# Optimization experiments

Measured on AMD Instinct MI355X. Metric: run time of the kernel, lower is better.

## Reference

```python
import jax, jax.numpy as jnp
import numpy as np

LR = 1e-4   # learning_rate from init
EPS = 1e-8


def setup_inputs() -> dict:
    key = jax.random.key(0)
    k1, k2 = jax.random.split(key)
    N, K, F = 8192, 8192, 4096
    return {
        "x": jax.random.normal(k1, (N, F), jnp.float32),
        "centroids": jax.random.normal(k2, (K, F), jnp.float32),
        "m": jnp.zeros((K,), jnp.float32),
        "v": jnp.zeros((K,), jnp.float32),
        "betas": jnp.array([0.9, 0.999, 1.0, 1.0], jnp.float32),
        "step": 1,
    }


def reference(x, centroids, m, v, betas, step):
    N = x.shape[0]
    K = centroids.shape[0]
    dt = x.dtype
    # dist[k, n] = ||x_n - c_k||^2, via norm expansion (same math as sum((x-c)^2))
    xn = jnp.sum(x * x, axis=1)                    # [N]
    cn = jnp.sum(centroids * centroids, axis=1)    # [K]
    dist = cn[:, None] + xn[None, :] - 2.0 * (centroids @ x.T)  # [K, N]
    nearest = jnp.argmin(dist, axis=0)             # [N]
    # point_loss = sum(dist[:, nearest]) / N ; sum over K of gathered cols == gather of colsums
    colsum = jnp.sum(dist, axis=0)                 # [N]
    point_loss = jnp.sum(colsum[nearest]) / N
    # sum_{i,j} ||c_i - c_j||^2 = 2K*sum||c||^2 - 2*||sum_i c_i||^2 (includes zero diagonal)
    csum = jnp.sum(centroids, axis=0)
    centroid_loss = 1.0 / (2.0 * K * jnp.sum(cn) - 2.0 * jnp.sum(csum * csum))
    # per-cluster segment reduce replaces the Python loop over K
    counts = jax.ops.segment_sum(jnp.ones((N,), dt), nearest, num_segments=K)  # [K]
    sums = jax.ops.segment_sum(x, nearest, num_segments=K)                     # [K, F]
    nonempty = counts > 0
    new_center = sums / jnp.maximum(counts, 1.0)[:, None]
    delta = jnp.where(nonempty, jnp.sum((new_center - centroids) ** 2, axis=1), 0.0)  # [K]
    delta_k = jnp.sum(nonempty.astype(dt))
    sum_delta = jnp.sum(delta)
    # Adam-style per-cluster state update (only for non-empty clusters)
    g = delta + betas[2] * point_loss + betas[3] * centroid_loss
    m_new = jnp.where(nonempty, betas[0] * m + (1.0 - betas[0]) * g, m)
    v_new = jnp.where(nonempty, betas[1] * v + (1.0 - betas[1]) * g * g, v)
    mh = m_new / (1.0 - betas[0] ** step)
    vh = v_new / (1.0 - betas[1] ** step)
    upd = LR * mh / (jnp.sqrt(vh) + EPS)
    next_centroids = jnp.where(nonempty[:, None], centroids - upd[:, None], centroids)
    return sum_delta / delta_k, point_loss, centroid_loss, next_centroids, m_new, v_new
```

## Files before the change

kernel.cpp:

```cpp
#include <hip/hip_runtime.h>
#include <stdint.h>

#define KCL 8192
#define NPT 8192
#define FD  4096
#define KF  33554432
#define LRC 1e-4f
#define EPSC 1e-8f
#define SLAB 1024
#define BK  32

typedef float  f32x4 __attribute__((ext_vector_type(4)));
typedef __fp16 h8    __attribute__((ext_vector_type(8)));
typedef __fp16 h4    __attribute__((ext_vector_type(4)));

struct Scal {
  float Scn;
  float csum2;
  float cl;
  float pl_sum;
  float sum_delta;
  int   nonempty;
};

__device__ __forceinline__ void gload16(const void* g, void* l) {
  __builtin_amdgcn_global_load_lds((const __attribute__((address_space(1))) void*)g,
                                   (__attribute__((address_space(3))) void*)l, 16, 0, 0);
}

__device__ __forceinline__ float wave_sum(float v) {
  #pragma unroll
  for (int m = 1; m < 64; m <<= 1) v += __shfl_xor(v, m, 64);
  return v;
}
__device__ __forceinline__ double wave_sum(double v) {
  #pragma unroll
  for (int m = 1; m < 64; m <<= 1) v += __shfl_xor(v, m, 64);
  return v;
}

__global__ __launch_bounds__(256) void rownorm_k(const float* __restrict__ src,
                                                 double* __restrict__ norms) {
  __shared__ double sred[4];
  const int r = blockIdx.x, t = threadIdx.x;
  const f32x4* row = (const f32x4*)(src + (size_t)r * FD);
  double ss = 0.0;
  #pragma unroll
  for (int q = 0; q < 4; ++q) {
    f32x4 v = row[q * 256 + t];
    ss += (double)(v[0]*v[0] + v[1]*v[1]) + (double)(v[2]*v[2] + v[3]*v[3]);
  }
  ss = wave_sum(ss);
  int wave = t >> 6, lane = t & 63;
  if (lane == 0) sred[wave] = ss;
  __syncthreads();
  if (t == 0) norms[r] = sred[0] + sred[1] + sred[2] + sred[3];
}

template<bool WITH_DOT>
__global__ __launch_bounds__(256) void prep_rows(
    const float* __restrict__ src, __fp16* __restrict__ hi, __fp16* __restrict__ lo,
    const float* __restrict__ csum, float* __restrict__ colsum, const Scal* __restrict__ sc)
{
  __shared__ double sred[4], sred2[4];
  const int r = blockIdx.x, t = threadIdx.x;
  const size_t rb = (size_t)r * FD;
  const f32x4* row = (const f32x4*)(src + rb);
  double ss = 0.0, dd = 0.0;
  #pragma unroll
  for (int q = 0; q < 4; ++q) {
    int c4 = q * 256 + t;
    f32x4 v = row[c4];
    h4 hv = __builtin_convertvector(v, h4);
    f32x4 hb = __builtin_convertvector(hv, f32x4);
    h4 lv = __builtin_convertvector(v - hb, h4);
    *(h4*)(hi + rb + (size_t)c4 * 4) = hv;
    *(h4*)(lo + rb + (size_t)c4 * 4) = lv;
    if (WITH_DOT) {
      ss += (double)(v[0]*v[0] + v[1]*v[1]) + (double)(v[2]*v[2] + v[3]*v[3]);
      f32x4 cs = *(const f32x4*)(csum + c4 * 4);
      dd += (double)(v[0]*cs[0] + v[1]*cs[1]) + (double)(v[2]*cs[2] + v[3]*cs[3]);
    }
  }
  if (WITH_DOT) {
    ss = wave_sum(ss); dd = wave_sum(dd);
    int wave = t >> 6, lane = t & 63;
    if (lane == 0) { sred[wave] = ss; sred2[wave] = dd; }
    __syncthreads();
    if (t == 0) {
      double S = sred[0] + sred[1] + sred[2] + sred[3];
      double D = sred2[0] + sred2[1] + sred2[2] + sred2[3];
      colsum[r] = (float)((double)sc->Scn + (double)KCL * S - 2.0 * D);
    }
  }
}

__global__ __launch_bounds__(256) void csum_part_k(const float* __restrict__ c,
                                                   float* __restrict__ parts) {
  int f = blockIdx.x * 256 + threadIdx.x;
  int r0 = blockIdx.y * 256;
  float s = 0.f;
  for (int i = 0; i < 256; ++i) s += c[(size_t)(r0 + i) * FD + f];
  parts[(size_t)blockIdx.y * FD + f] = s;
}

__global__ __launch_bounds__(256) void csum_reduce_k(const float* __restrict__ parts,
                                                     float* __restrict__ csum, Scal* sc) {
  int f = blockIdx.x * 256 + threadIdx.x;
  float s = 0.f;
  for (int j = 0; j < 32; ++j) s += parts[(size_t)j * FD + f];
  csum[f] = s;
  float sq = wave_sum(s * s);
  __shared__ float sr[4];
  int wave = threadIdx.x >> 6, lane = threadIdx.x & 63;
  if (lane == 0) sr[wave] = sq;
  __syncthreads();
  if (threadIdx.x == 0) atomicAdd(&sc->csum2, sr[0] + sr[1] + sr[2] + sr[3]);
}

__global__ __launch_bounds__(256) void cn_reduce_k(const double* __restrict__ cn, Scal* sc) {
  double s = 0.0;
  for (int i = threadIdx.x; i < KCL; i += 256) s += cn[i];
  s = wave_sum(s);
  __shared__ double sr[4];
  int wave = threadIdx.x >> 6, lane = threadIdx.x & 63;
  if (lane == 0) sr[wave] = s;
  __syncthreads();
  if (threadIdx.x == 0) {
    double S = sr[0] + sr[1] + sr[2] + sr[3];
    sc->Scn = (float)S;
    sc->cl = (float)(1.0 / (2.0 * (double)KCL * S - 2.0 * (double)sc->csum2));
  }
}

__global__ __launch_bounds__(512, 2) void gemm_argmin_k(
    const __fp16* __restrict__ Ahi, const __fp16* __restrict__ Alo,
    const __fp16* __restrict__ Bhi, const __fp16* __restrict__ Blo,
    const double* __restrict__ cn,
    double* __restrict__ part_val, int* __restrict__ part_idx,
    int kglob0, int nglob0, int swz)
{
  __shared__ __fp16 tile[2 * 4 * 8192];

  const int tid  = threadIdx.x;
  const int lane = tid & 63;
  const int w    = tid >> 6;
  const int wr   = w >> 2, wc = w & 3;
  const int ln15 = lane & 15, lc = lane >> 4;

  int kb, nb;
  if (swz) {
    int l = (blockIdx.x & 7) * 128 + (blockIdx.x >> 3);
    kb = l & 31; nb = l >> 5;
  } else {
    kb = blockIdx.y; nb = blockIdx.x;
  }
  const int k0l = kb * 256, n0l = nb * 256;
  const int k0g = kglob0 + k0l, n0g = nglob0 + n0l;

  const __fp16* gAh = Ahi + (size_t)k0l * FD;
  const __fp16* gAl = Alo + (size_t)k0l * FD;
  const __fp16* gBh = Bhi + (size_t)n0l * FD;
  const __fp16* gBl = Blo + (size_t)n0l * FD;

  const int c0 = tid,        r0 = c0 >> 2, sc0 = (c0 & 3) ^ ((r0 >> 1) & 3);
  const int c1 = tid + 512,  r1 = c1 >> 2, sc1 = (c1 & 3) ^ ((r1 >> 1) & 3);
  const size_t gof0 = (size_t)r0 * FD + sc0 * 8;
  const size_t gof1 = (size_t)r1 * FD + sc1 * 8;

  #define TBUF(buf, arr) (tile + (((buf) * 4 + (arr)) << 13))
  #define STAGE(gsrc, buf, arr, fo) do { \
    gload16((gsrc) + gof0 + (fo), TBUF(buf, arr) + c0 * 8); \
    gload16((gsrc) + gof1 + (fo), TBUF(buf, arr) + c1 * 8); } while (0)

  const int pcs = (lc ^ ((ln15 >> 1) & 3)) * 8;
  const int abase = wr * 128 + ln15;
  const int bbase = wc * 64 + ln15;

  f32x4 acc[8][4] = {};
  h8 ah[8], bh[4];

  STAGE(gAh, 0, 0, 0); STAGE(gBh, 0, 2, 0); STAGE(gAl, 0, 1, 0); STAGE(gBl, 0, 3, 0);
  asm volatile("s_waitcnt vmcnt(0)" ::: "memory");
  __builtin_amdgcn_s_barrier();

  for (int t = 0; t < FD / BK; ++t) {
    const int cur = t & 1, nxt = cur ^ 1;
    const size_t fo = (size_t)(t + 1) * BK;
    const bool st = (t < FD / BK - 1);

    {
      const __fp16* sA = TBUF(cur, 0);
      const __fp16* sB = TBUF(cur, 2);
      #pragma unroll
      for (int m = 0; m < 8; ++m) ah[m] = *(const h8*)(sA + (abase + m * 16) * 32 + pcs);
      #pragma unroll
      for (int n = 0; n < 4; ++n) bh[n] = *(const h8*)(sB + (bbase + n * 16) * 32 + pcs);
    }
    if (st) STAGE(gAh, nxt, 0, fo);
    __builtin_amdgcn_s_barrier();
    __builtin_amdgcn_s_setprio(1);
    #pragma unroll
    for (int m = 0; m < 8; ++m)
      #pragma unroll
      for (int n = 0; n < 4; ++n)
        acc[m][n] = __builtin_amdgcn_mfma_f32_16x16x32_f16(ah[m], bh[n], acc[m][n], 0, 0, 0);
    __builtin_amdgcn_s_setprio(0);
    asm volatile("s_waitcnt vmcnt(2)" ::: "memory");
    __builtin_amdgcn_sched_barrier(0);
    __builtin_amdgcn_s_barrier();

    {
      h8 bl[4];
      const __fp16* sB = TBUF(cur, 3);
      #pragma unroll
      for (int n = 0; n < 4; ++n) bl[n] = *(const h8*)(sB + (bbase + n * 16) * 32 + pcs);
      if (st) STAGE(gBh, nxt, 2, fo);
      __builtin_amdgcn_s_barrier();
      __builtin_amdgcn_s_setprio(1);
      #pragma unroll
      for (int m = 0; m < 8; ++m)
        #pragma unroll
        for (int n = 0; n < 4; ++n)
          acc[m][n] = __builtin_amdgcn_mfma_f32_16x16x32_f16(ah[m], bl[n], acc[m][n], 0, 0, 0);
      __builtin_amdgcn_s_setprio(0);
      __builtin_amdgcn_s_barrier();
    }

    {
      h8 al[8];
      const __fp16* sA = TBUF(cur, 1);
      #pragma unroll
      for (int m = 0; m < 8; ++m) al[m] = *(const h8*)(sA + (abase + m * 16) * 32 + pcs);
      if (st) { STAGE(gAl, nxt, 1, fo); STAGE(gBl, nxt, 3, fo); }
      __builtin_amdgcn_s_barrier();
      __builtin_amdgcn_s_setprio(1);
      #pragma unroll
      for (int m = 0; m < 8; ++m)
        #pragma unroll
        for (int n = 0; n < 4; ++n)
          acc[m][n] = __builtin_amdgcn_mfma_f32_16x16x32_f16(al[m], bh[n], acc[m][n], 0, 0, 0);
      __builtin_amdgcn_s_setprio(0);
      asm volatile("s_waitcnt vmcnt(4)" ::: "memory");
      __builtin_amdgcn_sched_barrier(0);
      __builtin_amdgcn_s_barrier();
    }
  }

  double* eCn = (double*)tile;
  double* eV  = (double*)(tile + 1024);
  int*    eI  = (int*)(tile + 3072);
  __syncthreads();
  if (tid < 256) eCn[tid] = cn[k0g + tid];
  __syncthreads();

  #pragma unroll
  for (int n = 0; n < 4; ++n) {
    double bv = 1e300; int bi = 0x7fffffff;
    #pragma unroll
    for (int m = 0; m < 8; ++m)
      #pragma unroll
      for (int j = 0; j < 4; ++j) {
        int kl = wr * 128 + m * 16 + lc * 4 + j;
        double d = eCn[kl] - 2.0 * (double)acc[m][n][j];
        if (d < bv || (d == bv && kl < bi)) { bv = d; bi = kl; }
      }
    #pragma unroll
    for (int mask = 16; mask < 64; mask <<= 1) {
      double ov = __shfl_xor(bv, mask, 64);
      int    oi = __shfl_xor(bi, mask, 64);
      if (ov < bv || (ov == bv && oi < bi)) { bv = ov; bi = oi; }
    }
    if (lc == 0) {
      int col = wc * 64 + n * 16 + ln15;
      eV[wr * 256 + col] = bv; eI[wr * 256 + col] = bi;
    }
  }
  __syncthreads();
  if (tid < 256) {
    double v0 = eV[tid]; int i0 = eI[tid];
    double v1 = eV[256 + tid]; int i1 = eI[256 + tid];
    if (v1 < v0 || (v1 == v0 && i1 < i0)) { v0 = v1; i0 = i1; }
    part_val[(size_t)(k0g >> 8) * NPT + n0g + tid] = v0;
    part_idx[(size_t)(k0g >> 8) * NPT + n0g + tid] = i0 + k0g;
  }
  #undef TBUF
  #undef STAGE
}

__global__ __launch_bounds__(256) void nearest_k(
    const double* __restrict__ part_val, const int* __restrict__ part_idx,
    const float* __restrict__ colsum, int* __restrict__ nearest,
    int* __restrict__ counts, Scal* sc)
{
  int n = blockIdx.x * 256 + threadIdx.x;
  double bv = 1e300; int bi = 0x7fffffff;
  for (int kb = 0; kb < 32; ++kb) {
    double v = part_val[(size_t)kb * NPT + n];
    int    i = part_idx[(size_t)kb * NPT + n];
    if (v < bv || (v == bv && i < bi)) { bv = v; bi = i; }
  }
  nearest[n] = bi;
  atomicAdd(&counts[bi], 1);
  float pls = wave_sum(colsum[bi]);
  __shared__ float sr[4];
  int wave = threadIdx.x >> 6, lane = threadIdx.x & 63;
  if (lane == 0) sr[wave] = pls;
  __syncthreads();
  if (threadIdx.x == 0) atomicAdd(&sc->pl_sum, sr[0] + sr[1] + sr[2] + sr[3]);
}

__global__ __launch_bounds__(256) void scan_k(const int* __restrict__ counts,
                                              int* __restrict__ offsets) {
  __shared__ int s[256];
  int t = threadIdx.x;
  int base = t * 32;
  int sum = 0;
  for (int i = 0; i < 32; ++i) sum += counts[base + i];
  s[t] = sum; __syncthreads();
  for (int off = 1; off < 256; off <<= 1) {
    int v = (t >= off) ? s[t - off] : 0;
    __syncthreads();
    s[t] += v;
    __syncthreads();
  }
  int run = s[t] - sum;
  for (int i = 0; i < 32; ++i) { offsets[base + i] = run; run += counts[base + i]; }
}

__global__ __launch_bounds__(256) void fill_k(const int* __restrict__ nearest,
                                              const int* __restrict__ offsets,
                                              int* __restrict__ cursor, int* __restrict__ list) {
  int n = blockIdx.x * 256 + threadIdx.x;
  int k = nearest[n];
  int p = atomicAdd(&cursor[k], 1);
  list[offsets[k] + p] = n;
}

__global__ __launch_bounds__(256) void cluster_k(
    const float* __restrict__ x, const float* __restrict__ cen,
    const int* __restrict__ counts, const int* __restrict__ offsets,
    const int* __restrict__ list, float* __restrict__ delta, Scal* sc)
{
  int k = blockIdx.x, t = threadIdx.x;
  int cnt = counts[k];
  if (cnt == 0) { if (t == 0) delta[k] = 0.f; return; }
  f32x4 acc[4] = {};
  int off = offsets[k];
  for (int i = 0; i < cnt; ++i) {
    int n = list[off + i];
    const f32x4* row = (const f32x4*)(x + (size_t)n * FD);
    #pragma unroll
    for (int q = 0; q < 4; ++q) acc[q] += row[q * 256 + t];
  }
  const f32x4* crow = (const f32x4*)(cen + (size_t)k * FD);
  float part = 0.f;
  float fc = (float)cnt;
  #pragma unroll
  for (int q = 0; q < 4; ++q) {
    f32x4 c4 = crow[q * 256 + t];
    #pragma unroll
    for (int j = 0; j < 4; ++j) {
      float d = acc[q][j] / fc - c4[j];
      part += d * d;
    }
  }
  part = wave_sum(part);
  __shared__ float sr[4];
  int wave = t >> 6, lane = t & 63;
  if (lane == 0) sr[wave] = part;
  __syncthreads();
  if (t == 0) {
    float dsum = sr[0] + sr[1] + sr[2] + sr[3];
    delta[k] = dsum;
    atomicAdd(&sc->sum_delta, dsum);
    atomicAdd(&sc->nonempty, 1);
  }
}

__global__ __launch_bounds__(256) void adam_k(
    const float* __restrict__ m_in, const float* __restrict__ v_in,
    const float* __restrict__ betas, const int* __restrict__ step,
    const int* __restrict__ counts, const float* __restrict__ delta,
    const Scal* __restrict__ sc, float* __restrict__ out, float* __restrict__ upd)
{
  int k = blockIdx.x * 256 + threadIdx.x;
  float b0 = betas[0], b1 = betas[1], b2 = betas[2], b3 = betas[3];
  float pl = sc->pl_sum / (float)NPT;
  float cl = sc->cl;
  bool ne = counts[k] > 0;
  float g = delta[k] + b2 * pl + b3 * cl;
  float mn = ne ? (b0 * m_in[k] + (1.f - b0) * g) : m_in[k];
  float vn = ne ? (b1 * v_in[k] + (1.f - b1) * g * g) : v_in[k];
  int st = *step;
  float mh = mn / (1.f - powf(b0, (float)st));
  float vh = vn / (1.f - powf(b1, (float)st));
  float u = LRC * mh / (sqrtf(vh) + EPSC);
  upd[k] = ne ? u : 0.f;
  out[3 + (size_t)KF + k] = mn;
  out[3 + (size_t)KF + KCL + k] = vn;
  if (k == 0) {
    out[0] = sc->sum_delta / (float)sc->nonempty;
    out[1] = pl;
    out[2] = cl;
  }
}

__global__ __launch_bounds__(256) void nextc_k(const float* __restrict__ cen,
                                               const float* __restrict__ upd,
                                               float* __restrict__ out) {
  int i4 = blockIdx.x * 256 + threadIdx.x;
  f32x4 c = *(const f32x4*)(cen + (size_t)i4 * 4);
  float u = upd[i4 >> 10];
  float* o = out + 3 + (size_t)i4 * 4;
  o[0] = c[0] - u; o[1] = c[1] - u; o[2] = c[2] - u; o[3] = c[3] - u;
}

extern "C" void kernel_launch(void* const* d_in, const int* in_sizes, int n_in,
                              void* d_out, int out_size, void* d_ws, size_t ws_size,
                              hipStream_t stream) {
  const float* x     = (const float*)d_in[0];
  const float* cen   = (const float*)d_in[1];
  const float* m_in  = (const float*)d_in[2];
  const float* v_in  = (const float*)d_in[3];
  const float* betas = (const float*)d_in[4];
  const int*   step  = (const int*)d_in[5];
  float* out = (float*)d_out;

  char* p = (char*)d_ws;
  auto alloc = [&](size_t b) { char* r = p; p += (b + 255) & ~(size_t)255; return r; };
  Scal* sc      = (Scal*)alloc(sizeof(Scal));
  int* counts   = (int*)alloc(KCL * 4);
  int* cursor   = (int*)alloc(KCL * 4);
  size_t zlen   = (size_t)(p - (char*)d_ws);
  int* offsets  = (int*)alloc(KCL * 4);
  int* list     = (int*)alloc(NPT * 4);
  int* nearest  = (int*)alloc(NPT * 4);
  double* cn    = (double*)alloc(KCL * 8);
  float* colsum = (float*)alloc(NPT * 4);
  float* delta  = (float*)alloc(KCL * 4);
  float* upd    = (float*)alloc(KCL * 4);
  float* csum   = (float*)alloc(FD * 4);
  float* cparts = (float*)alloc(32 * FD * 4);
  double* pval  = (double*)alloc((size_t)32 * NPT * 8);
  int*   pidx   = (int*)alloc((size_t)32 * NPT * 4);
  const bool fast = ws_size >= (size_t)280 * 1024 * 1024;
  const size_t splitRows = fast ? (size_t)KCL : (size_t)SLAB;
  __fp16* chi = (__fp16*)alloc(splitRows * FD * 2);
  __fp16* clo = (__fp16*)alloc(splitRows * FD * 2);
  __fp16* xhi = (__fp16*)alloc(splitRows * FD * 2);
  __fp16* xlo = (__fp16*)alloc(splitRows * FD * 2);
  (void)in_sizes; (void)n_in; (void)out_size;

  hipMemsetAsync(d_ws, 0, zlen, stream);

  rownorm_k<<<KCL, 256, 0, stream>>>(cen, cn);
  csum_part_k<<<dim3(16, 32), 256, 0, stream>>>(cen, cparts);
  csum_reduce_k<<<16, 256, 0, stream>>>(cparts, csum, sc);
  cn_reduce_k<<<1, 256, 0, stream>>>(cn, sc);

  if (fast) {
    prep_rows<false><<<KCL, 256, 0, stream>>>(cen, chi, clo, nullptr, nullptr, nullptr);
    prep_rows<true><<<NPT, 256, 0, stream>>>(x, xhi, xlo, csum, colsum, sc);
    gemm_argmin_k<<<1024, 512, 0, stream>>>(chi, clo, xhi, xlo, cn, pval, pidx, 0, 0, 1);
  } else {
    for (int q = 0; q < NPT / SLAB; ++q) {
      prep_rows<true><<<SLAB, 256, 0, stream>>>(x + (size_t)q * SLAB * FD, xhi, xlo,
                                                csum, colsum + q * SLAB, sc);
      for (int pp = 0; pp < KCL / SLAB; ++pp) {
        prep_rows<false><<<SLAB, 256, 0, stream>>>(cen + (size_t)pp * SLAB * FD, chi, clo,
                                                   nullptr, nullptr, nullptr);
        gemm_argmin_k<<<dim3(SLAB / 256, SLAB / 256), 512, 0, stream>>>(
            chi, clo, xhi, xlo, cn, pval, pidx, pp * SLAB, q * SLAB, 0);
      }
    }
  }

  nearest_k<<<NPT / 256, 256, 0, stream>>>(pval, pidx, colsum, nearest, counts, sc);
  scan_k<<<1, 256, 0, stream>>>(counts, offsets);
  fill_k<<<NPT / 256, 256, 0, stream>>>(nearest, offsets, cursor, list);
  cluster_k<<<KCL, 256, 0, stream>>>(x, cen, counts, offsets, list, delta, sc);
  adam_k<<<KCL / 256, 256, 0, stream>>>(m_in, v_in, betas, step, counts, delta, sc, out, upd);
  nextc_k<<<KF / 4 / 256, 256, 0, stream>>>(cen, upd, out);
}
```

Measured before the change: 1.801 ms.

## Use 32x32 MFMA in GEMM, fuse centroid prep and cluster/Adam/update kernels

Switches the split-fp16 GEMM from 16x16x32 to 32x32x16 MFMA tiles, which lowers LDS fragment reads per flop and simplifies the argmin cross-lane reduction. It also fuses centroid row norms, column partial sums and the hi/lo fp16 split into a single pass over the centroids. The cluster mean, Adam update and next-centroid write are merged into one per-cluster kernel, removing the delta/upd buffers and two extra passes over 128MB. The price is a larger accumulator layout per wave, a more serial 32-row loop per block in the prep kernel, and an extra tiny finalize launch.

```diff
diff --git a/kernel.cpp b/kernel.cpp
--- a/kernel.cpp
+++ b/kernel.cpp
@@ -10,9 +10,10 @@
 #define SLAB 1024
 #define BK  32
 
-typedef float  f32x4 __attribute__((ext_vector_type(4)));
-typedef __fp16 h8    __attribute__((ext_vector_type(8)));
-typedef __fp16 h4    __attribute__((ext_vector_type(4)));
+typedef float  f32x4  __attribute__((ext_vector_type(4)));
+typedef float  f32x16 __attribute__((ext_vector_type(16)));
+typedef __fp16 h8     __attribute__((ext_vector_type(8)));
+typedef __fp16 h4     __attribute__((ext_vector_type(4)));
 
 struct Scal {
   float Scn;
@@ -37,6 +38,41 @@
   #pragma unroll
   for (int m = 1; m < 64; m <<= 1) v += __shfl_xor(v, m, 64);
   return v;
+}
+
+__global__ __launch_bounds__(256) void prep_cen_k(
+    const float* __restrict__ src, __fp16* __restrict__ hi, __fp16* __restrict__ lo,
+    double* __restrict__ norms, float* __restrict__ parts)
+{
+  __shared__ double snorm[32][4];
+  const int t = threadIdx.x;
+  const int wv = t >> 6, lane = t & 63;
+  const int rbase = blockIdx.x * 32;
+  f32x4 cs[4] = {};
+  for (int r = 0; r < 32; ++r) {
+    const size_t rb = (size_t)(rbase + r) * FD;
+    const f32x4* row = (const f32x4*)(src + rb);
+    double ss = 0.0;
+    #pragma unroll
+    for (int q = 0; q < 4; ++q) {
+      int c4i = q * 256 + t;
+      f32x4 v = row[c4i];
+      h4 hv = __builtin_convertvector(v, h4);
+      f32x4 hb = __builtin_convertvector(hv, f32x4);
+      h4 lv = __builtin_convertvector(v - hb, h4);
+      *(h4*)(hi + rb + (size_t)c4i * 4) = hv;
+      *(h4*)(lo + rb + (size_t)c4i * 4) = lv;
+      ss += (double)(v[0]*v[0] + v[1]*v[1]) + (double)(v[2]*v[2] + v[3]*v[3]);
+      cs[q] += v;
+    }
+    double wsum = wave_sum(ss);
+    if (lane == 0) snorm[r][wv] = wsum;
+  }
+  __syncthreads();
+  if (t < 32) norms[rbase + t] = snorm[t][0] + snorm[t][1] + snorm[t][2] + snorm[t][3];
+  #pragma unroll
+  for (int q = 0; q < 4; ++q)
+    *(f32x4*)(parts + (size_t)blockIdx.x * FD + (size_t)(q * 256 + t) * 4) = cs[q];
 }
 
 __global__ __launch_bounds__(256) void rownorm_k(const float* __restrict__ src,
@@ -105,10 +141,11 @@
 }
 
 __global__ __launch_bounds__(256) void csum_reduce_k(const float* __restrict__ parts,
-                                                     float* __restrict__ csum, Scal* sc) {
+                                                     float* __restrict__ csum, Scal* sc,
+                                                     int nparts) {
   int f = blockIdx.x * 256 + threadIdx.x;
   float s = 0.f;
-  for (int j = 0; j < 32; ++j) s += parts[(size_t)j * FD + f];
+  for (int j = 0; j < nparts; ++j) s += parts[(size_t)j * FD + f];
   csum[f] = s;
   float sq = wave_sum(s * s);
   __shared__ float sr[4];
@@ -146,7 +183,7 @@
   const int lane = tid & 63;
   const int w    = tid >> 6;
   const int wr   = w >> 2, wc = w & 3;
-  const int ln15 = lane & 15, lc = lane >> 4;
+  const int l31  = lane & 31, l5 = lane >> 5;
 
   int kb, nb;
   if (swz) {
@@ -173,12 +210,15 @@
     gload16((gsrc) + gof0 + (fo), TBUF(buf, arr) + c0 * 8); \
     gload16((gsrc) + gof1 + (fo), TBUF(buf, arr) + c1 * 8); } while (0)
 
-  const int pcs = (lc ^ ((ln15 >> 1) & 3)) * 8;
-  const int abase = wr * 128 + ln15;
-  const int bbase = wc * 64 + ln15;
-
-  f32x4 acc[8][4] = {};
-  h8 ah[8], bh[4];
+  const int arow0 = wr * 128 + l31;
+  const int brow0 = wc * 64 + l31;
+  const int rxa = (arow0 >> 1) & 3;
+  const int rxb = (brow0 >> 1) & 3;
+  const int pA[2] = { ((0 + l5) ^ rxa) * 8, ((2 + l5) ^ rxa) * 8 };
+  const int pB[2] = { ((0 + l5) ^ rxb) * 8, ((2 + l5) ^ rxb) * 8 };
+
+  f32x16 acc[4][2] = {};
+  h8 ah[4][2], bh[2][2];
 
   STAGE(gAh, 0, 0, 0); STAGE(gBh, 0, 2, 0); STAGE(gAl, 0, 1, 0); STAGE(gBl, 0, 3, 0);
   asm volatile("s_waitcnt vmcnt(0)" ::: "memory");
@@ -193,53 +233,71 @@
       const __fp16* sA = TBUF(cur, 0);
       const __fp16* sB = TBUF(cur, 2);
       #pragma unroll
-      for (int m = 0; m < 8; ++m) ah[m] = *(const h8*)(sA + (abase + m * 16) * 32 + pcs);
-      #pragma unroll
-      for (int n = 0; n < 4; ++n) bh[n] = *(const h8*)(sB + (bbase + n * 16) * 32 + pcs);
+      for (int m = 0; m < 4; ++m) {
+        ah[m][0] = *(const h8*)(sA + (arow0 + m * 32) * 32 + pA[0]);
+        ah[m][1] = *(const h8*)(sA + (arow0 + m * 32) * 32 + pA[1]);
+      }
+      #pragma unroll
+      for (int n = 0; n < 2; ++n) {
+        bh[n][0] = *(const h8*)(sB + (brow0 + n * 32) * 32 + pB[0]);
+        bh[n][1] = *(const h8*)(sB + (brow0 + n * 32) * 32 + pB[1]);
+      }
     }
     if (st) STAGE(gAh, nxt, 0, fo);
     __builtin_amdgcn_s_barrier();
     __builtin_amdgcn_s_setprio(1);
     #pragma unroll
-    for (int m = 0; m < 8; ++m)
-      #pragma unroll
-      for (int n = 0; n < 4; ++n)
-        acc[m][n] = __builtin_amdgcn_mfma_f32_16x16x32_f16(ah[m], bh[n], acc[m][n], 0, 0, 0);
+    for (int ks = 0; ks < 2; ++ks)
+      #pragma unroll
+      for (int m = 0; m < 4; ++m)
+        #pragma unroll
+        for (int n = 0; n < 2; ++n)
+          acc[m][n] = __builtin_amdgcn_mfma_f32_32x32x16_f16(ah[m][ks], bh[n][ks], acc[m][n], 0, 0, 0);
     __builtin_amdgcn_s_setprio(0);
     asm volatile("s_waitcnt vmcnt(2)" ::: "memory");
     __builtin_amdgcn_sched_barrier(0);
     __builtin_amdgcn_s_barrier();
 
     {
-      h8 bl[4];
+      h8 bl[2][2];
       const __fp16* sB = TBUF(cur, 3);
       #pragma unroll
-      for (int n = 0; n < 4; ++n) bl[n] = *(const h8*)(sB + (bbase + n * 16) * 32 + pcs);
+      for (int n = 0; n < 2; ++n) {
+        bl[n][0] = *(const h8*)(sB + (brow0 + n * 32) * 32 + pB[0]);
+        bl[n][1] = *(const h8*)(sB + (brow0 + n * 32) * 32 + pB[1]);
+      }
       if (st) STAGE(gBh, nxt, 2, fo);
       __builtin_amdgcn_s_barrier();
       __builtin_amdgcn_s_setprio(1);
       #pragma unroll
-      for (int m = 0; m < 8; ++m)
+      for (int ks = 0; ks < 2; ++ks)
         #pragma unroll
-        for (int n = 0; n < 4; ++n)
-          acc[m][n] = __builtin_amdgcn_mfma_f32_16x16x32_f16(ah[m], bl[n], acc[m][n], 0, 0, 0);
+        for (int m = 0; m < 4; ++m)
+          #pragma unroll
+          for (int n = 0; n < 2; ++n)
+            acc[m][n] = __builtin_amdgcn_mfma_f32_32x32x16_f16(ah[m][ks], bl[n][ks], acc[m][n], 0, 0, 0);
       __builtin_amdgcn_s_setprio(0);
       __builtin_amdgcn_s_barrier();
     }
 
     {
-      h8 al[8];
+      h8 al[4][2];
       const __fp16* sA = TBUF(cur, 1);
       #pragma unroll
-      for (int m = 0; m < 8; ++m) al[m] = *(const h8*)(sA + (abase + m * 16) * 32 + pcs);
+      for (int m = 0; m < 4; ++m) {
+        al[m][0] = *(const h8*)(sA + (arow0 + m * 32) * 32 + pA[0]);
+        al[m][1] = *(const h8*)(sA + (arow0 + m * 32) * 32 + pA[1]);
+      }
       if (st) { STAGE(gAl, nxt, 1, fo); STAGE(gBl, nxt, 3, fo); }
       __builtin_amdgcn_s_barrier();
       __builtin_amdgcn_s_setprio(1);
       #pragma unroll
-      for (int m = 0; m < 8; ++m)
+      for (int ks = 0; ks < 2; ++ks)
         #pragma unroll
-        for (int n = 0; n < 4; ++n)
-          acc[m][n] = __builtin_amdgcn_mfma_f32_16x16x32_f16(al[m], bh[n], acc[m][n], 0, 0, 0);
+        for (int m = 0; m < 4; ++m)
+          #pragma unroll
+          for (int n = 0; n < 2; ++n)
+            acc[m][n] = __builtin_amdgcn_mfma_f32_32x32x16_f16(al[m][ks], bh[n][ks], acc[m][n], 0, 0, 0);
       __builtin_amdgcn_s_setprio(0);
       asm volatile("s_waitcnt vmcnt(4)" ::: "memory");
       __builtin_amdgcn_sched_barrier(0);
@@ -255,24 +313,21 @@
   __syncthreads();
 
   #pragma unroll
-  for (int n = 0; n < 4; ++n) {
+  for (int n = 0; n < 2; ++n) {
     double bv = 1e300; int bi = 0x7fffffff;
     #pragma unroll
-    for (int m = 0; m < 8; ++m)
-      #pragma unroll
-      for (int j = 0; j < 4; ++j) {
-        int kl = wr * 128 + m * 16 + lc * 4 + j;
-        double d = eCn[kl] - 2.0 * (double)acc[m][n][j];
+    for (int m = 0; m < 4; ++m)
+      #pragma unroll
+      for (int reg = 0; reg < 16; ++reg) {
+        int kl = wr * 128 + m * 32 + (reg & 3) + 8 * (reg >> 2) + 4 * l5;
+        double d = eCn[kl] - 2.0 * (double)acc[m][n][reg];
         if (d < bv || (d == bv && kl < bi)) { bv = d; bi = kl; }
       }
-    #pragma unroll
-    for (int mask = 16; mask < 64; mask <<= 1) {
-      double ov = __shfl_xor(bv, mask, 64);
-      int    oi = __shfl_xor(bi, mask, 64);
-      if (ov < bv || (ov == bv && oi < bi)) { bv = ov; bi = oi; }
-    }
-    if (lc == 0) {
-      int col = wc * 64 + n * 16 + ln15;
+    double ov = __shfl_xor(bv, 32, 64);
+    int    oi = __shfl_xor(bi, 32, 64);
+    if (ov < bv || (ov == bv && oi < bi)) { bv = ov; bi = oi; }
+    if (l5 == 0) {
+      int col = wc * 64 + n * 32 + l31;
       eV[wr * 256 + col] = bv; eI[wr * 256 + col] = bi;
     }
   }
@@ -337,83 +392,81 @@
   list[offsets[k] + p] = n;
 }
 
-__global__ __launch_bounds__(256) void cluster_k(
+__global__ __launch_bounds__(256) void cluster_adam_k(
     const float* __restrict__ x, const float* __restrict__ cen,
-    const int* __restrict__ counts, const int* __restrict__ offsets,
-    const int* __restrict__ list, float* __restrict__ delta, Scal* sc)
-{
-  int k = blockIdx.x, t = threadIdx.x;
-  int cnt = counts[k];
-  if (cnt == 0) { if (t == 0) delta[k] = 0.f; return; }
-  f32x4 acc[4] = {};
-  int off = offsets[k];
-  for (int i = 0; i < cnt; ++i) {
-    int n = list[off + i];
-    const f32x4* row = (const f32x4*)(x + (size_t)n * FD);
-    #pragma unroll
-    for (int q = 0; q < 4; ++q) acc[q] += row[q * 256 + t];
-  }
-  const f32x4* crow = (const f32x4*)(cen + (size_t)k * FD);
-  float part = 0.f;
-  float fc = (float)cnt;
-  #pragma unroll
-  for (int q = 0; q < 4; ++q) {
-    f32x4 c4 = crow[q * 256 + t];
-    #pragma unroll
-    for (int j = 0; j < 4; ++j) {
-      float d = acc[q][j] / fc - c4[j];
-      part += d * d;
-    }
-  }
-  part = wave_sum(part);
-  __shared__ float sr[4];
-  int wave = t >> 6, lane = t & 63;
-  if (lane == 0) sr[wave] = part;
-  __syncthreads();
-  if (t == 0) {
-    float dsum = sr[0] + sr[1] + sr[2] + sr[3];
-    delta[k] = dsum;
-    atomicAdd(&sc->sum_delta, dsum);
-    atomicAdd(&sc->nonempty, 1);
-  }
-}
-
-__global__ __launch_bounds__(256) void adam_k(
     const float* __restrict__ m_in, const float* __restrict__ v_in,
     const float* __restrict__ betas, const int* __restrict__ step,
-    const int* __restrict__ counts, const float* __restrict__ delta,
-    const Scal* __restrict__ sc, float* __restrict__ out, float* __restrict__ upd)
+    const int* __restrict__ counts, const int* __restrict__ offsets,
+    const int* __restrict__ list, Scal* sc, float* __restrict__ out)
 {
-  int k = blockIdx.x * 256 + threadIdx.x;
-  float b0 = betas[0], b1 = betas[1], b2 = betas[2], b3 = betas[3];
-  float pl = sc->pl_sum / (float)NPT;
-  float cl = sc->cl;
-  bool ne = counts[k] > 0;
-  float g = delta[k] + b2 * pl + b3 * cl;
-  float mn = ne ? (b0 * m_in[k] + (1.f - b0) * g) : m_in[k];
-  float vn = ne ? (b1 * v_in[k] + (1.f - b1) * g * g) : v_in[k];
-  int st = *step;
-  float mh = mn / (1.f - powf(b0, (float)st));
-  float vh = vn / (1.f - powf(b1, (float)st));
-  float u = LRC * mh / (sqrtf(vh) + EPSC);
-  upd[k] = ne ? u : 0.f;
-  out[3 + (size_t)KF + k] = mn;
-  out[3 + (size_t)KF + KCL + k] = vn;
-  if (k == 0) {
-    out[0] = sc->sum_delta / (float)sc->nonempty;
-    out[1] = pl;
-    out[2] = cl;
-  }
-}
-
-__global__ __launch_bounds__(256) void nextc_k(const float* __restrict__ cen,
-                                               const float* __restrict__ upd,
-                                               float* __restrict__ out) {
-  int i4 = blockIdx.x * 256 + threadIdx.x;
-  f32x4 c = *(const f32x4*)(cen + (size_t)i4 * 4);
-  float u = upd[i4 >> 10];
-  float* o = out + 3 + (size_t)i4 * 4;
-  o[0] = c[0] - u; o[1] = c[1] - u; o[2] = c[2] - u; o[3] = c[3] - u;
+  const int k = blockIdx.x, t = threadIdx.x;
+  const int cnt = counts[k];
+  const size_t kb = (size_t)k * FD;
+  const f32x4* crow = (const f32x4*)(cen + kb);
+  f32x4 c4[4];
+  #pragma unroll
+  for (int q = 0; q < 4; ++q) c4[q] = crow[q * 256 + t];
+
+  float mn, vn, u;
+  if (cnt > 0) {
+    f32x4 acc[4] = {};
+    const int off = offsets[k];
+    for (int i = 0; i < cnt; ++i) {
+      const f32x4* row = (const f32x4*)(x + (size_t)list[off + i] * FD);
+      #pragma unroll
+      for (int q = 0; q < 4; ++q) acc[q] += row[q * 256 + t];
+    }
+    float part = 0.f;
+    const float fc = (float)cnt;
+    #pragma unroll
+    for (int q = 0; q < 4; ++q)
+      #pragma unroll
+      for (int j = 0; j < 4; ++j) {
+        float d = acc[q][j] / fc - c4[q][j];
+        part += d * d;
+      }
+    part = wave_sum(part);
+    __shared__ float sr[4];
+    __shared__ float sdelta;
+    int wave = t >> 6, lane = t & 63;
+    if (lane == 0) sr[wave] = part;
+    __syncthreads();
+    if (t == 0) {
+      float dsum = sr[0] + sr[1] + sr[2] + sr[3];
+      sdelta = dsum;
+      atomicAdd(&sc->sum_delta, dsum);
+      atomicAdd(&sc->nonempty, 1);
+    }
+    __syncthreads();
+    float delta_k = sdelta;
+    float b0 = betas[0], b1 = betas[1], b2 = betas[2], b3 = betas[3];
+    float pl = sc->pl_sum / (float)NPT;
+    float g = delta_k + b2 * pl + b3 * sc->cl;
+    mn = b0 * m_in[k] + (1.f - b0) * g;
+    vn = b1 * v_in[k] + (1.f - b1) * g * g;
+    int st = *step;
+    float mh = mn / (1.f - powf(b0, (float)st));
+    float vh = vn / (1.f - powf(b1, (float)st));
+    u = LRC * mh / (sqrtf(vh) + EPSC);
+  } else {
+    mn = m_in[k]; vn = v_in[k]; u = 0.f;
+  }
+  if (t == 0) {
+    out[3 + (size_t)KF + k] = mn;
+    out[3 + (size_t)KF + KCL + k] = vn;
+  }
+  float* orow = out + 3 + kb;
+  #pragma unroll
+  for (int q = 0; q < 4; ++q) {
+    f32x4 o = c4[q] - u;
+    *(f32x4*)(orow + (size_t)(q * 256 + t) * 4) = o;
+  }
+}
+
+__global__ void finalize_k(const Scal* __restrict__ sc, float* __restrict__ out) {
+  out[0] = sc->sum_delta / (float)sc->nonempty;
+  out[1] = sc->pl_sum / (float)NPT;
+  out[2] = sc->cl;
 }
 
 extern "C" void kernel_launch(void* const* d_in, const int* in_sizes, int n_in,
@@ -438,10 +491,8 @@
   int* nearest  = (int*)alloc(NPT * 4);
   double* cn    = (double*)alloc(KCL * 8);
   float* colsum = (float*)alloc(NPT * 4);
-  float* delta  = (float*)alloc(KCL * 4);
-  float* upd    = (float*)alloc(KCL * 4);
   float* csum   = (float*)alloc(FD * 4);
-  float* cparts = (float*)alloc(32 * FD * 4);
+  float* cparts = (float*)alloc((size_t)256 * FD * 4);
   double* pval  = (double*)alloc((size_t)32 * NPT * 8);
   int*   pidx   = (int*)alloc((size_t)32 * NPT * 4);
   const bool fast = ws_size >= (size_t)280 * 1024 * 1024;
@@ -454,16 +505,17 @@
 
   hipMemsetAsync(d_ws, 0, zlen, stream);
 
-  rownorm_k<<<KCL, 256, 0, stream>>>(cen, cn);
-  csum_part_k<<<dim3(16, 32), 256, 0, stream>>>(cen, cparts);
-  csum_reduce_k<<<16, 256, 0, stream>>>(cparts, csum, sc);
-  cn_reduce_k<<<1, 256, 0, stream>>>(cn, sc);
-
   if (fast) {
-    prep_rows<false><<<KCL, 256, 0, stream>>>(cen, chi, clo, nullptr, nullptr, nullptr);
+    prep_cen_k<<<256, 256, 0, stream>>>(cen, chi, clo, cn, cparts);
+    csum_reduce_k<<<16, 256, 0, stream>>>(cparts, csum, sc, 256);
+    cn_reduce_k<<<1, 256, 0, stream>>>(cn, sc);
     prep_rows<true><<<NPT, 256, 0, stream>>>(x, xhi, xlo, csum, colsum, sc);
     gemm_argmin_k<<<1024, 512, 0, stream>>>(chi, clo, xhi, xlo, cn, pval, pidx, 0, 0, 1);
   } else {
+    rownorm_k<<<KCL, 256, 0, stream>>>(cen, cn);
+    csum_part_k<<<dim3(16, 32), 256, 0, stream>>>(cen, cparts);
+    csum_reduce_k<<<16, 256, 0, stream>>>(cparts, csum, sc, 32);
+    cn_reduce_k<<<1, 256, 0, stream>>>(cn, sc);
     for (int q = 0; q < NPT / SLAB; ++q) {
       prep_rows<true><<<SLAB, 256, 0, stream>>>(x + (size_t)q * SLAB * FD, xhi, xlo,
                                                 csum, colsum + q * SLAB, sc);
@@ -479,7 +531,7 @@
   nearest_k<<<NPT / 256, 256, 0, stream>>>(pval, pidx, colsum, nearest, counts, sc);
   scan_k<<<1, 256, 0, stream>>>(counts, offsets);
   fill_k<<<NPT / 256, 256, 0, stream>>>(nearest, offsets, cursor, list);
-  cluster_k<<<KCL, 256, 0, stream>>>(x, cen, counts, offsets, list, delta, sc);
-  adam_k<<<KCL / 256, 256, 0, stream>>>(m_in, v_in, betas, step, counts, delta, sc, out, upd);
-  nextc_k<<<KF / 4 / 256, 256, 0, stream>>>(cen, upd, out);
-}
+  cluster_adam_k<<<KCL, 256, 0, stream>>>(x, cen, m_in, v_in, betas, step,
+                                          counts, offsets, list, sc, out);
+  finalize_k<<<1, 1, 0, stream>>>(sc, out);
+}
```

After: 1.995 ms. 10.8% more time.

## Fuse cluster, Adam and next-centroid kernels; trim GEMM barriers and retile swizzle

Applied to the files above, without the earlier changes.

Merges the per-cluster delta reduction, the Adam state update and the next-centroid write into one kernel per cluster, with a tiny finalize kernel for the scalar outputs. This avoids the extra launches and a second full read of the centroid matrix. The GEMM main loop also loses several workgroup barriers between the LDS fragment reads and the MFMA phases, and its block swizzle changes so each XCD gets a 16x2 block of tiles for better L2 reuse. Removing barriers risks LDS read/write races on the double-buffered tiles if the remaining waits do not cover them.

```diff
diff --git a/kernel.cpp b/kernel.cpp
--- a/kernel.cpp
+++ b/kernel.cpp
@@ -105,10 +105,11 @@
 }
 
 __global__ __launch_bounds__(256) void csum_reduce_k(const float* __restrict__ parts,
-                                                     float* __restrict__ csum, Scal* sc) {
+                                                     float* __restrict__ csum, Scal* sc,
+                                                     int nparts) {
   int f = blockIdx.x * 256 + threadIdx.x;
   float s = 0.f;
-  for (int j = 0; j < 32; ++j) s += parts[(size_t)j * FD + f];
+  for (int j = 0; j < nparts; ++j) s += parts[(size_t)j * FD + f];
   csum[f] = s;
   float sq = wave_sum(s * s);
   __shared__ float sr[4];
@@ -150,8 +151,10 @@
 
   int kb, nb;
   if (swz) {
-    int l = (blockIdx.x & 7) * 128 + (blockIdx.x >> 3);
-    kb = l & 31; nb = l >> 5;
+    int xcd = blockIdx.x & 7, idx = blockIdx.x >> 3;
+    int st = idx >> 5, i = idx & 31;
+    kb = (st & 1) * 16 + (i & 15);
+    nb = (st >> 1) * 16 + xcd * 2 + (i >> 4);
   } else {
     kb = blockIdx.y; nb = blockIdx.x;
   }
@@ -198,7 +201,6 @@
       for (int n = 0; n < 4; ++n) bh[n] = *(const h8*)(sB + (bbase + n * 16) * 32 + pcs);
     }
     if (st) STAGE(gAh, nxt, 0, fo);
-    __builtin_amdgcn_s_barrier();
     __builtin_amdgcn_s_setprio(1);
     #pragma unroll
     for (int m = 0; m < 8; ++m)
@@ -206,7 +208,8 @@
       for (int n = 0; n < 4; ++n)
         acc[m][n] = __builtin_amdgcn_mfma_f32_16x16x32_f16(ah[m], bh[n], acc[m][n], 0, 0, 0);
     __builtin_amdgcn_s_setprio(0);
-    asm volatile("s_waitcnt vmcnt(2)" ::: "memory");
+    if (st) asm volatile("s_waitcnt vmcnt(2)" ::: "memory");
+    else    asm volatile("s_waitcnt vmcnt(0)" ::: "memory");
     __builtin_amdgcn_sched_barrier(0);
     __builtin_amdgcn_s_barrier();
 
@@ -216,7 +219,6 @@
       #pragma unroll
       for (int n = 0; n < 4; ++n) bl[n] = *(const h8*)(sB + (bbase + n * 16) * 32 + pcs);
       if (st) STAGE(gBh, nxt, 2, fo);
-      __builtin_amdgcn_s_barrier();
       __builtin_amdgcn_s_setprio(1);
       #pragma unroll
       for (int m = 0; m < 8; ++m)
@@ -224,7 +226,6 @@
         for (int n = 0; n < 4; ++n)
           acc[m][n] = __builtin_amdgcn_mfma_f32_16x16x32_f16(ah[m], bl[n], acc[m][n], 0, 0, 0);
       __builtin_amdgcn_s_setprio(0);
-      __builtin_amdgcn_s_barrier();
     }
 
     {
@@ -233,7 +234,6 @@
       #pragma unroll
       for (int m = 0; m < 8; ++m) al[m] = *(const h8*)(sA + (abase + m * 16) * 32 + pcs);
       if (st) { STAGE(gAl, nxt, 1, fo); STAGE(gBl, nxt, 3, fo); }
-      __builtin_amdgcn_s_barrier();
       __builtin_amdgcn_s_setprio(1);
       #pragma unroll
       for (int m = 0; m < 8; ++m)
@@ -337,83 +337,81 @@
   list[offsets[k] + p] = n;
 }
 
-__global__ __launch_bounds__(256) void cluster_k(
+__global__ __launch_bounds__(256) void cluster_adam_k(
     const float* __restrict__ x, const float* __restrict__ cen,
-    const int* __restrict__ counts, const int* __restrict__ offsets,
-    const int* __restrict__ list, float* __restrict__ delta, Scal* sc)
-{
-  int k = blockIdx.x, t = threadIdx.x;
-  int cnt = counts[k];
-  if (cnt == 0) { if (t == 0) delta[k] = 0.f; return; }
-  f32x4 acc[4] = {};
-  int off = offsets[k];
-  for (int i = 0; i < cnt; ++i) {
-    int n = list[off + i];
-    const f32x4* row = (const f32x4*)(x + (size_t)n * FD);
-    #pragma unroll
-    for (int q = 0; q < 4; ++q) acc[q] += row[q * 256 + t];
-  }
-  const f32x4* crow = (const f32x4*)(cen + (size_t)k * FD);
-  float part = 0.f;
-  float fc = (float)cnt;
-  #pragma unroll
-  for (int q = 0; q < 4; ++q) {
-    f32x4 c4 = crow[q * 256 + t];
-    #pragma unroll
-    for (int j = 0; j < 4; ++j) {
-      float d = acc[q][j] / fc - c4[j];
-      part += d * d;
-    }
-  }
-  part = wave_sum(part);
-  __shared__ float sr[4];
-  int wave = t >> 6, lane = t & 63;
-  if (lane == 0) sr[wave] = part;
-  __syncthreads();
-  if (t == 0) {
-    float dsum = sr[0] + sr[1] + sr[2] + sr[3];
-    delta[k] = dsum;
-    atomicAdd(&sc->sum_delta, dsum);
-    atomicAdd(&sc->nonempty, 1);
-  }
-}
-
-__global__ __launch_bounds__(256) void adam_k(
     const float* __restrict__ m_in, const float* __restrict__ v_in,
     const float* __restrict__ betas, const int* __restrict__ step,
-    const int* __restrict__ counts, const float* __restrict__ delta,
-    const Scal* __restrict__ sc, float* __restrict__ out, float* __restrict__ upd)
+    const int* __restrict__ counts, const int* __restrict__ offsets,
+    const int* __restrict__ list, Scal* sc, float* __restrict__ out)
 {
-  int k = blockIdx.x * 256 + threadIdx.x;
-  float b0 = betas[0], b1 = betas[1], b2 = betas[2], b3 = betas[3];
-  float pl = sc->pl_sum / (float)NPT;
-  float cl = sc->cl;
-  bool ne = counts[k] > 0;
-  float g = delta[k] + b2 * pl + b3 * cl;
-  float mn = ne ? (b0 * m_in[k] + (1.f - b0) * g) : m_in[k];
-  float vn = ne ? (b1 * v_in[k] + (1.f - b1) * g * g) : v_in[k];
-  int st = *step;
-  float mh = mn / (1.f - powf(b0, (float)st));
-  float vh = vn / (1.f - powf(b1, (float)st));
-  float u = LRC * mh / (sqrtf(vh) + EPSC);
-  upd[k] = ne ? u : 0.f;
-  out[3 + (size_t)KF + k] = mn;
-  out[3 + (size_t)KF + KCL + k] = vn;
-  if (k == 0) {
-    out[0] = sc->sum_delta / (float)sc->nonempty;
-    out[1] = pl;
-    out[2] = cl;
-  }
-}
-
-__global__ __launch_bounds__(256) void nextc_k(const float* __restrict__ cen,
-                                               const float* __restrict__ upd,
-                                               float* __restrict__ out) {
-  int i4 = blockIdx.x * 256 + threadIdx.x;
-  f32x4 c = *(const f32x4*)(cen + (size_t)i4 * 4);
-  float u = upd[i4 >> 10];
-  float* o = out + 3 + (size_t)i4 * 4;
-  o[0] = c[0] - u; o[1] = c[1] - u; o[2] = c[2] - u; o[3] = c[3] - u;
+  const int k = blockIdx.x, t = threadIdx.x;
+  const int cnt = counts[k];
+  const size_t kb = (size_t)k * FD;
+  const f32x4* crow = (const f32x4*)(cen + kb);
+  f32x4 c4[4];
+  #pragma unroll
+  for (int q = 0; q < 4; ++q) c4[q] = crow[q * 256 + t];
+
+  float mn, vn, u;
+  if (cnt > 0) {
+    f32x4 acc[4] = {};
+    const int off = offsets[k];
+    for (int i = 0; i < cnt; ++i) {
+      const f32x4* row = (const f32x4*)(x + (size_t)list[off + i] * FD);
+      #pragma unroll
+      for (int q = 0; q < 4; ++q) acc[q] += row[q * 256 + t];
+    }
+    float part = 0.f;
+    const float fc = (float)cnt;
+    #pragma unroll
+    for (int q = 0; q < 4; ++q)
+      #pragma unroll
+      for (int j = 0; j < 4; ++j) {
+        float d = acc[q][j] / fc - c4[q][j];
+        part += d * d;
+      }
+    part = wave_sum(part);
+    __shared__ float sr[4];
+    __shared__ float sdelta;
+    int wave = t >> 6, lane = t & 63;
+    if (lane == 0) sr[wave] = part;
+    __syncthreads();
+    if (t == 0) {
+      float dsum = sr[0] + sr[1] + sr[2] + sr[3];
+      sdelta = dsum;
+      atomicAdd(&sc->sum_delta, dsum);
+      atomicAdd(&sc->nonempty, 1);
+    }
+    __syncthreads();
+    float delta_k = sdelta;
+    float b0 = betas[0], b1 = betas[1], b2 = betas[2], b3 = betas[3];
+    float pl = sc->pl_sum / (float)NPT;
+    float g = delta_k + b2 * pl + b3 * sc->cl;
+    mn = b0 * m_in[k] + (1.f - b0) * g;
+    vn = b1 * v_in[k] + (1.f - b1) * g * g;
+    int st = *step;
+    float mh = mn / (1.f - powf(b0, (float)st));
+    float vh = vn / (1.f - powf(b1, (float)st));
+    u = LRC * mh / (sqrtf(vh) + EPSC);
+  } else {
+    mn = m_in[k]; vn = v_in[k]; u = 0.f;
+  }
+  if (t == 0) {
+    out[3 + (size_t)KF + k] = mn;
+    out[3 + (size_t)KF + KCL + k] = vn;
+  }
+  float* orow = out + 3 + kb;
+  #pragma unroll
+  for (int q = 0; q < 4; ++q) {
+    f32x4 o = c4[q] - u;
+    *(f32x4*)(orow + (size_t)(q * 256 + t) * 4) = o;
+  }
+}
+
+__global__ void finalize_k(const Scal* __restrict__ sc, float* __restrict__ out) {
+  out[0] = sc->sum_delta / (float)sc->nonempty;
+  out[1] = sc->pl_sum / (float)NPT;
+  out[2] = sc->cl;
 }
 
 extern "C" void kernel_launch(void* const* d_in, const int* in_sizes, int n_in,
@@ -438,10 +436,8 @@
   int* nearest  = (int*)alloc(NPT * 4);
   double* cn    = (double*)alloc(KCL * 8);
   float* colsum = (float*)alloc(NPT * 4);
-  float* delta  = (float*)alloc(KCL * 4);
-  float* upd    = (float*)alloc(KCL * 4);
   float* csum   = (float*)alloc(FD * 4);
-  float* cparts = (float*)alloc(32 * FD * 4);
+  float* cparts = (float*)alloc((size_t)32 * FD * 4);
   double* pval  = (double*)alloc((size_t)32 * NPT * 8);
   int*   pidx   = (int*)alloc((size_t)32 * NPT * 4);
   const bool fast = ws_size >= (size_t)280 * 1024 * 1024;
@@ -456,7 +452,7 @@
 
   rownorm_k<<<KCL, 256, 0, stream>>>(cen, cn);
   csum_part_k<<<dim3(16, 32), 256, 0, stream>>>(cen, cparts);
-  csum_reduce_k<<<16, 256, 0, stream>>>(cparts, csum, sc);
+  csum_reduce_k<<<16, 256, 0, stream>>>(cparts, csum, sc, 32);
   cn_reduce_k<<<1, 256, 0, stream>>>(cn, sc);
 
   if (fast) {
@@ -479,7 +475,7 @@
   nearest_k<<<NPT / 256, 256, 0, stream>>>(pval, pidx, colsum, nearest, counts, sc);
   scan_k<<<1, 256, 0, stream>>>(counts, offsets);
   fill_k<<<NPT / 256, 256, 0, stream>>>(nearest, offsets, cursor, list);
-  cluster_k<<<KCL, 256, 0, stream>>>(x, cen, counts, offsets, list, delta, sc);
-  adam_k<<<KCL / 256, 256, 0, stream>>>(m_in, v_in, betas, step, counts, delta, sc, out, upd);
-  nextc_k<<<KF / 4 / 256, 256, 0, stream>>>(cen, upd, out);
-}
+  cluster_adam_k<<<KCL, 256, 0, stream>>>(x, cen, m_in, v_in, betas, step,
+                                          counts, offsets, list, sc, out);
+  finalize_k<<<1, 1, 0, stream>>>(sc, out);
+}
```

New measurement: 1.663 ms. 1.08x faster.
